# Optimization experiments

Measured on AMD Instinct MI355X. Metric: run time of the kernel, lower is better.

## Reference

```python
import jax, jax.numpy as jnp
import numpy as np
from jax import lax

B, H = 32768, 32  # batch, hidden_dim (hidden_dim=32 fixed by the source module)
T = 128           # num_steps


def setup_inputs() -> dict:
    key = jax.random.key(0)
    ks = jax.random.split(key, 8)
    s = 1.0 / np.sqrt(H)  # torch default uniform(-1/sqrt(H), 1/sqrt(H)) scale
    return {
        "in_data": jax.random.normal(ks[0], (B, H), dtype=jnp.float32),
        "hidden": jax.random.normal(ks[1], (B, H), dtype=jnp.float32),
        "W_ih": jax.random.uniform(ks[2], (3 * H, H), jnp.float32, -s, s),
        "W_hh": jax.random.uniform(ks[3], (3 * H, H), jnp.float32, -s, s),
        "b_ih": jax.random.uniform(ks[4], (3 * H,), jnp.float32, -s, s),
        "b_hh": jax.random.uniform(ks[5], (3 * H,), jnp.float32, -s, s),
        "W_out": jax.random.uniform(ks[6], (1, H), jnp.float32, -s, s),
        "b_out": jax.random.uniform(ks[7], (1,), jnp.float32, -s, s),
        "num_steps": T,
    }


def reference(in_data, hidden, W_ih, W_hh, b_ih, b_hh, W_out, b_out, num_steps):
    # the GRU hidden output is fed back as the next step's input.
    def gru_cell(x, h):
        gi = x @ W_ih.T + b_ih  # [B, 3H]
        gh = h @ W_hh.T + b_hh  # [B, 3H]
        i_r, i_z, i_n = jnp.split(gi, 3, axis=-1)
        h_r, h_z, h_n = jnp.split(gh, 3, axis=-1)
        r = jax.nn.sigmoid(i_r + h_r)
        z = jax.nn.sigmoid(i_z + h_z)
        n = jnp.tanh(i_n + r * h_n)
        return (1.0 - z) * n + z * h

    def step(carry, _):
        x, h = carry
        h_new = gru_cell(x, h)
        y = h_new @ W_out.T + b_out  # [B, 1]
        return (h_new, h_new), y[:, 0]

    _, ys = lax.scan(step, (in_data, hidden), None, length=num_steps)  # ys: [T, B]
    return ys.T  # [B, T], matching torch's stack().squeeze(2).permute(1,0)
```

## Files before the change

### kernel.cpp

```cpp
#include <hip/hip_runtime.h>


typedef __attribute__((ext_vector_type(8)))  short short8;
typedef __attribute__((ext_vector_type(4)))  float f32x4;

struct F3 { short8 h, m, l; };

__device__ __forceinline__ void ldrow8(const float* p, float f[8]) {
    f32x4 a = *(const f32x4*)p;
    f32x4 b = *(const f32x4*)(p + 4);
    f[0]=a[0]; f[1]=a[1]; f[2]=a[2]; f[3]=a[3];
    f[4]=b[0]; f[5]=b[1]; f[6]=b[2]; f[7]=b[3];
}

__device__ __forceinline__ F3 split8(const float f[8]) {
    unsigned H[8], M[8], L[8];
    #pragma unroll
    for (int i = 0; i < 8; ++i) {
        unsigned a = __float_as_uint(f[i]);
        unsigned h = a & 0xffff0000u;
        float    t = f[i] - __uint_as_float(h);
        unsigned m = __float_as_uint(t) & 0xffff0000u;
        float    u = t - __uint_as_float(m);
        unsigned l = __float_as_uint(u) & 0xffff0000u;
        H[i] = h; M[i] = m; L[i] = l;
    }
    union { unsigned u[4]; short8 s; } uh, um, ul;
    #pragma unroll
    for (int p = 0; p < 4; ++p) {
        uh.u[p] = __builtin_amdgcn_perm(H[2*p+1], H[2*p], 0x07060302u);
        um.u[p] = __builtin_amdgcn_perm(M[2*p+1], M[2*p], 0x07060302u);
        ul.u[p] = __builtin_amdgcn_perm(L[2*p+1], L[2*p], 0x07060302u);
    }
    F3 r; r.h = uh.s; r.m = um.s; r.l = ul.s; return r;
}

#define MFMA(a,b,c) __builtin_amdgcn_mfma_f32_16x16x32_bf16((a),(b),(c),0,0,0)

__device__ __forceinline__ f32x4 mm6(const F3& A, const F3& B, f32x4 c) {
    c = MFMA(A.h, B.l, c);
    c = MFMA(A.l, B.h, c);
    c = MFMA(A.m, B.m, c);
    c = MFMA(A.h, B.m, c);
    c = MFMA(A.m, B.h, c);
    c = MFMA(A.h, B.h, c);
    return c;
}

__device__ __forceinline__ float rcp_nr(float x) {
    float r = __builtin_amdgcn_rcpf(x);
    return r * fmaf(-x, r, 2.f);
}
__device__ __forceinline__ float sigm_(float x) {
    x = __builtin_amdgcn_fmed3f(x, -60.f, 60.f);
    return rcp_nr(1.f + __expf(-x));
}
__device__ __forceinline__ float tanh_(float x) {
    x = __builtin_amdgcn_fmed3f(x, -30.f, 30.f);
    return fmaf(-2.f, rcp_nr(__expf(2.f * x) + 1.f), 1.f);
}
__device__ __forceinline__ float comb_(float ar, float az, float an_, float ahn, float hp) {
    float rr = sigm_(ar);
    float zz = sigm_(az);
    float nn = tanh_(fmaf(rr, ahn, an_));
    return fmaf(zz, hp - nn, nn);
}

__global__ __launch_bounds__(256, 2)
void gru_mfma(const float* __restrict__ in_data, const float* __restrict__ hidden,
              const float* __restrict__ W_ih,   const float* __restrict__ W_hh,
              const float* __restrict__ b_ih,   const float* __restrict__ b_hh,
              const float* __restrict__ W_out,  const float* __restrict__ b_out,
              float* __restrict__ out, int B, int T)
{
    const int tid  = threadIdx.x;
    const int lane = tid & 63, wv = tid >> 6;
    const int n    = lane & 15;
    const int g    = lane >> 4;
    const int k0   = g * 8;
    const long e   = (long)blockIdx.x * 64 + wv * 16 + n;

    const int rlo = 8 * (n >> 2) + (n & 3);
    const int rhi = rlo + 4;

    f32x4 bC[8];
    #pragma unroll
    for (int p = 0; p < 2; ++p) {
        #pragma unroll
        for (int r = 0; r < 4; ++r) {
            const int c = 8 * g + 4 * p + r;
            bC[0 + p][r] = b_ih[c]      + b_hh[c];
            bC[2 + p][r] = b_ih[32 + c] + b_hh[32 + c];
            bC[4 + p][r] = b_ih[64 + c];
            bC[6 + p][r] = b_hh[64 + c];
        }
    }
    float wl[4], wh[4];
    #pragma unroll
    for (int r = 0; r < 4; ++r) { wl[r] = W_out[8*g + r]; wh[r] = W_out[8*g + 4 + r]; }
    const float boutv = b_out[0];
    float* const op = out + e * (long)T;

    float hp[8];
    F3 Bv, Bx;
    {
        float f[8]; ldrow8(hidden + e * 32 + k0, f);
        #pragma unroll
        for (int i = 0; i < 8; ++i) hp[i] = f[i];
        Bv = split8(f);
        float fx[8]; ldrow8(in_data + e * 32 + k0, fx);
        Bx = split8(fx);
    }

    F3 A[8];
    f32x4 C[8];

    #pragma unroll
    for (int gs = 0; gs < 3; ++gs) {
        float fl[8], fh[8];
        ldrow8(W_ih + (gs * 32 + rlo) * 32 + k0, fl);
        ldrow8(W_ih + (gs * 32 + rhi) * 32 + k0, fh);
        A[2*gs] = split8(fl); A[2*gs+1] = split8(fh);
    }
    #pragma unroll
    for (int rt = 0; rt < 6; ++rt) C[rt] = mm6(A[rt], Bx, bC[rt]);

    #pragma unroll
    for (int gs = 0; gs < 3; ++gs) {
        float fl[8], fh[8];
        ldrow8(W_hh + (gs * 32 + rlo) * 32 + k0, fl);
        ldrow8(W_hh + (gs * 32 + rhi) * 32 + k0, fh);
        A[2*gs] = split8(fl); A[2*gs+1] = split8(fh);
    }
    #pragma unroll
    for (int rt = 0; rt < 4; ++rt) C[rt] = mm6(A[rt], Bv, C[rt]);
    C[6] = mm6(A[4], Bv, bC[6]);
    C[7] = mm6(A[5], Bv, bC[7]);

    #pragma unroll
    for (int gs = 0; gs < 2; ++gs) {
        float fl[8], fh[8], g2[8];
        ldrow8(W_ih + (gs * 32 + rlo) * 32 + k0, fl);
        ldrow8(W_hh + (gs * 32 + rlo) * 32 + k0, g2);
        #pragma unroll
        for (int i = 0; i < 8; ++i) fl[i] += g2[i];
        ldrow8(W_ih + (gs * 32 + rhi) * 32 + k0, fh);
        ldrow8(W_hh + (gs * 32 + rhi) * 32 + k0, g2);
        #pragma unroll
        for (int i = 0; i < 8; ++i) fh[i] += g2[i];
        A[2*gs] = split8(fl); A[2*gs+1] = split8(fh);
    }
    {
        float fl[8], fh[8];
        ldrow8(W_ih + (64 + rlo) * 32 + k0, fl);
        ldrow8(W_ih + (64 + rhi) * 32 + k0, fh);
        A[4] = split8(fl); A[5] = split8(fh);
        ldrow8(W_hh + (64 + rlo) * 32 + k0, fl);
        ldrow8(W_hh + (64 + rhi) * 32 + k0, fh);
        A[6] = split8(fl); A[7] = split8(fh);
    }

    #pragma unroll 1
    for (int t = 0; t < T; ++t) {
        float h8[8], yp = 0.f;
        #pragma unroll
        for (int r = 0; r < 4; ++r) {
            float a  = comb_(C[0][r], C[2][r], C[4][r], C[6][r], hp[r]);
            float b2 = comb_(C[1][r], C[3][r], C[5][r], C[7][r], hp[4 + r]);
            yp = fmaf(wl[r], a,  yp);
            yp = fmaf(wh[r], b2, yp);
            h8[r] = a; h8[4 + r] = b2;
            hp[r] = a; hp[4 + r] = b2;
        }
        yp += __shfl_xor(yp, 16);
        yp += __shfl_xor(yp, 32);
        if (lane < 16) op[t] = yp + boutv;
        if (t == T - 1) break;

        Bv = split8(h8);
        #pragma unroll
        for (int rt = 0; rt < 8; ++rt) C[rt] = mm6(A[rt], Bv, bC[rt]);
    }
}

extern "C" void kernel_launch(void* const* d_in, const int* in_sizes, int n_in,
                              void* d_out, int out_size, void* d_ws, size_t ws_size,
                              hipStream_t stream) {
    const float* in_data = (const float*)d_in[0];
    const float* hidden  = (const float*)d_in[1];
    const float* W_ih    = (const float*)d_in[2];
    const float* W_hh    = (const float*)d_in[3];
    const float* b_ih    = (const float*)d_in[4];
    const float* b_hh    = (const float*)d_in[5];
    const float* W_out   = (const float*)d_in[6];
    const float* b_out   = (const float*)d_in[7];
    float* out = (float*)d_out;

    const int B = in_sizes[0] / 32;
    const int T = out_size / B;
    const int blocks = B / 64;

    gru_mfma<<<blocks, 256, 0, stream>>>(in_data, hidden, W_ih, W_hh,
                                         b_ih, b_hh, W_out, b_out, out, B, T);
}
```

Before: 298.8 us.

## Interleave two batch groups per wave to overlap MFMA with gate math

Each wave now processes two 16-row batch groups, A and B. The recurrent MFMA chain for one group is interleaved with the sigmoid/tanh combine of the other, so the matrix and vector units can overlap instead of serialising on the per-step dependency. The log2e scaling is folded into the weights and biases, letting the gates use raw exp2 without a multiply or clamp. Blocks shrink to one wave with launch_bounds(64,1), which changes the occupancy and register budget, and dropping the clamps risks inf/NaN-adjacent edge behaviour on extreme inputs.

Result: faster. 290.1 us (-2.9%).

```diff
diff --git a/kernel.cpp b/kernel.cpp
--- a/kernel.cpp
+++ b/kernel.cpp
@@ -11,6 +11,11 @@
     f32x4 b = *(const f32x4*)(p + 4);
     f[0]=a[0]; f[1]=a[1]; f[2]=a[2]; f[3]=a[3];
     f[4]=b[0]; f[5]=b[1]; f[6]=b[2]; f[7]=b[3];
+}
+__device__ __forceinline__ void ldrow8s(const float* p, float f[8], float s) {
+    ldrow8(p, f);
+    #pragma unroll
+    for (int i = 0; i < 8; ++i) f[i] *= s;
 }
 
 __device__ __forceinline__ F3 split8(const float f[8]) {
@@ -47,38 +52,59 @@
     return c;
 }
 
+__device__ __forceinline__ void mfma8(const F3 A[8], const F3& Bv,
+                                      const f32x4 bC[8], f32x4 C[8]) {
+    #pragma unroll
+    for (int rt = 0; rt < 8; ++rt) C[rt] = mm6(A[rt], Bv, bC[rt]);
+}
+
 __device__ __forceinline__ float rcp_nr(float x) {
     float r = __builtin_amdgcn_rcpf(x);
     return r * fmaf(-x, r, 2.f);
 }
-__device__ __forceinline__ float sigm_(float x) {
-    x = __builtin_amdgcn_fmed3f(x, -60.f, 60.f);
-    return rcp_nr(1.f + __expf(-x));
-}
-__device__ __forceinline__ float tanh_(float x) {
-    x = __builtin_amdgcn_fmed3f(x, -30.f, 30.f);
-    return fmaf(-2.f, rcp_nr(__expf(2.f * x) + 1.f), 1.f);
-}
-__device__ __forceinline__ float comb_(float ar, float az, float an_, float ahn, float hp) {
-    float rr = sigm_(ar);
-    float zz = sigm_(az);
-    float nn = tanh_(fmaf(rr, ahn, an_));
+__device__ __forceinline__ float comb_(float arN, float azN, float anS, float ahnS, float hp) {
+    float rr = rcp_nr(1.f + __builtin_amdgcn_exp2f(arN));
+    float zz = rcp_nr(1.f + __builtin_amdgcn_exp2f(azN));
+    float q  = rcp_nr(__builtin_amdgcn_exp2f(fmaf(rr, ahnS, anS)) + 1.f);
+    float nn = fmaf(-2.f, q, 1.f);
     return fmaf(zz, hp - nn, nn);
 }
 
-__global__ __launch_bounds__(256, 2)
+__device__ __forceinline__ void combineG(const f32x4 C[8], float hp[8], F3& Bv,
+                                         const float wl[4], const float wh[4],
+                                         float boutv, float* op, int t, bool st) {
+    float h8[8], yp = 0.f;
+    #pragma unroll
+    for (int r = 0; r < 4; ++r) {
+        float a  = comb_(C[0][r], C[2][r], C[4][r], C[6][r], hp[r]);
+        float b2 = comb_(C[1][r], C[3][r], C[5][r], C[7][r], hp[4 + r]);
+        yp = fmaf(wl[r], a, yp);
+        yp = fmaf(wh[r], b2, yp);
+        h8[r] = a; h8[4 + r] = b2;
+        hp[r] = a; hp[4 + r] = b2;
+    }
+    yp += __shfl_xor(yp, 16);
+    yp += __shfl_xor(yp, 32);
+    if (st) op[t] = yp + boutv;
+    Bv = split8(h8);
+}
+
+__global__ __launch_bounds__(64, 1)
 void gru_mfma(const float* __restrict__ in_data, const float* __restrict__ hidden,
               const float* __restrict__ W_ih,   const float* __restrict__ W_hh,
               const float* __restrict__ b_ih,   const float* __restrict__ b_hh,
               const float* __restrict__ W_out,  const float* __restrict__ b_out,
               float* __restrict__ out, int B, int T)
 {
-    const int tid  = threadIdx.x;
-    const int lane = tid & 63, wv = tid >> 6;
+    const float S_RZ = -1.44269504088896340736f;
+    const float S_N  =  2.88539008177792681472f;
+
+    const int lane = threadIdx.x & 63;
     const int n    = lane & 15;
     const int g    = lane >> 4;
     const int k0   = g * 8;
-    const long e   = (long)blockIdx.x * 64 + wv * 16 + n;
+    const long eA  = (long)blockIdx.x * 32 + n;
+    const long eB  = eA + 16;
 
     const int rlo = 8 * (n >> 2) + (n & 3);
     const int rhi = rlo + 4;
@@ -89,53 +115,63 @@
         #pragma unroll
         for (int r = 0; r < 4; ++r) {
             const int c = 8 * g + 4 * p + r;
-            bC[0 + p][r] = b_ih[c]      + b_hh[c];
-            bC[2 + p][r] = b_ih[32 + c] + b_hh[32 + c];
-            bC[4 + p][r] = b_ih[64 + c];
-            bC[6 + p][r] = b_hh[64 + c];
+            bC[0 + p][r] = S_RZ * (b_ih[c]      + b_hh[c]);
+            bC[2 + p][r] = S_RZ * (b_ih[32 + c] + b_hh[32 + c]);
+            bC[4 + p][r] = S_N  *  b_ih[64 + c];
+            bC[6 + p][r] = S_N  *  b_hh[64 + c];
         }
     }
     float wl[4], wh[4];
     #pragma unroll
     for (int r = 0; r < 4; ++r) { wl[r] = W_out[8*g + r]; wh[r] = W_out[8*g + 4 + r]; }
     const float boutv = b_out[0];
-    float* const op = out + e * (long)T;
-
-    float hp[8];
-    F3 Bv, Bx;
+    float* const opA = out + eA * (long)T;
+    float* const opB = out + eB * (long)T;
+
+    float hpA[8], hpB[8];
+    F3 BvA, BvB, BxA, BxB;
     {
-        float f[8]; ldrow8(hidden + e * 32 + k0, f);
-        #pragma unroll
-        for (int i = 0; i < 8; ++i) hp[i] = f[i];
-        Bv = split8(f);
-        float fx[8]; ldrow8(in_data + e * 32 + k0, fx);
-        Bx = split8(fx);
+        float f[8];
+        ldrow8(hidden + eA * 32 + k0, f);
+        #pragma unroll
+        for (int i = 0; i < 8; ++i) hpA[i] = f[i];
+        BvA = split8(f);
+        ldrow8(hidden + eB * 32 + k0, f);
+        #pragma unroll
+        for (int i = 0; i < 8; ++i) hpB[i] = f[i];
+        BvB = split8(f);
+        ldrow8(in_data + eA * 32 + k0, f); BxA = split8(f);
+        ldrow8(in_data + eB * 32 + k0, f); BxB = split8(f);
     }
 
     F3 A[8];
-    f32x4 C[8];
+    f32x4 CA[8], CB[8];
 
     #pragma unroll
     for (int gs = 0; gs < 3; ++gs) {
+        const float s = (gs < 2) ? S_RZ : S_N;
         float fl[8], fh[8];
-        ldrow8(W_ih + (gs * 32 + rlo) * 32 + k0, fl);
-        ldrow8(W_ih + (gs * 32 + rhi) * 32 + k0, fh);
+        ldrow8s(W_ih + (gs * 32 + rlo) * 32 + k0, fl, s);
+        ldrow8s(W_ih + (gs * 32 + rhi) * 32 + k0, fh, s);
         A[2*gs] = split8(fl); A[2*gs+1] = split8(fh);
     }
     #pragma unroll
-    for (int rt = 0; rt < 6; ++rt) C[rt] = mm6(A[rt], Bx, bC[rt]);
+    for (int rt = 0; rt < 6; ++rt) { CA[rt] = mm6(A[rt], BxA, bC[rt]);
+                                     CB[rt] = mm6(A[rt], BxB, bC[rt]); }
 
     #pragma unroll
     for (int gs = 0; gs < 3; ++gs) {
+        const float s = (gs < 2) ? S_RZ : S_N;
         float fl[8], fh[8];
-        ldrow8(W_hh + (gs * 32 + rlo) * 32 + k0, fl);
-        ldrow8(W_hh + (gs * 32 + rhi) * 32 + k0, fh);
+        ldrow8s(W_hh + (gs * 32 + rlo) * 32 + k0, fl, s);
+        ldrow8s(W_hh + (gs * 32 + rhi) * 32 + k0, fh, s);
         A[2*gs] = split8(fl); A[2*gs+1] = split8(fh);
     }
     #pragma unroll
-    for (int rt = 0; rt < 4; ++rt) C[rt] = mm6(A[rt], Bv, C[rt]);
-    C[6] = mm6(A[4], Bv, bC[6]);
-    C[7] = mm6(A[5], Bv, bC[7]);
+    for (int rt = 0; rt < 4; ++rt) { CA[rt] = mm6(A[rt], BvA, CA[rt]);
+                                     CB[rt] = mm6(A[rt], BvB, CB[rt]); }
+    CA[6] = mm6(A[4], BvA, bC[6]);  CB[6] = mm6(A[4], BvB, bC[6]);
+    CA[7] = mm6(A[5], BvA, bC[7]);  CB[7] = mm6(A[5], BvB, bC[7]);
 
     #pragma unroll
     for (int gs = 0; gs < 2; ++gs) {
@@ -143,44 +179,36 @@
         ldrow8(W_ih + (gs * 32 + rlo) * 32 + k0, fl);
         ldrow8(W_hh + (gs * 32 + rlo) * 32 + k0, g2);
         #pragma unroll
-        for (int i = 0; i < 8; ++i) fl[i] += g2[i];
+        for (int i = 0; i < 8; ++i) fl[i] = S_RZ * (fl[i] + g2[i]);
         ldrow8(W_ih + (gs * 32 + rhi) * 32 + k0, fh);
         ldrow8(W_hh + (gs * 32 + rhi) * 32 + k0, g2);
         #pragma unroll
-        for (int i = 0; i < 8; ++i) fh[i] += g2[i];
+        for (int i = 0; i < 8; ++i) fh[i] = S_RZ * (fh[i] + g2[i]);
         A[2*gs] = split8(fl); A[2*gs+1] = split8(fh);
     }
     {
         float fl[8], fh[8];
-        ldrow8(W_ih + (64 + rlo) * 32 + k0, fl);
-        ldrow8(W_ih + (64 + rhi) * 32 + k0, fh);
+        ldrow8s(W_ih + (64 + rlo) * 32 + k0, fl, S_N);
+        ldrow8s(W_ih + (64 + rhi) * 32 + k0, fh, S_N);
         A[4] = split8(fl); A[5] = split8(fh);
-        ldrow8(W_hh + (64 + rlo) * 32 + k0, fl);
-        ldrow8(W_hh + (64 + rhi) * 32 + k0, fh);
+        ldrow8s(W_hh + (64 + rlo) * 32 + k0, fl, S_N);
+        ldrow8s(W_hh + (64 + rhi) * 32 + k0, fh, S_N);
         A[6] = split8(fl); A[7] = split8(fh);
     }
 
+    const bool st = (lane < 16);
+
+    combineG(CA, hpA, BvA, wl, wh, boutv, opA, 0, st);
+
     #pragma unroll 1
-    for (int t = 0; t < T; ++t) {
-        float h8[8], yp = 0.f;
-        #pragma unroll
-        for (int r = 0; r < 4; ++r) {
-            float a  = comb_(C[0][r], C[2][r], C[4][r], C[6][r], hp[r]);
-            float b2 = comb_(C[1][r], C[3][r], C[5][r], C[7][r], hp[4 + r]);
-            yp = fmaf(wl[r], a,  yp);
-            yp = fmaf(wh[r], b2, yp);
-            h8[r] = a; h8[4 + r] = b2;
-            hp[r] = a; hp[4 + r] = b2;
-        }
-        yp += __shfl_xor(yp, 16);
-        yp += __shfl_xor(yp, 32);
-        if (lane < 16) op[t] = yp + boutv;
-        if (t == T - 1) break;
-
-        Bv = split8(h8);
-        #pragma unroll
-        for (int rt = 0; rt < 8; ++rt) C[rt] = mm6(A[rt], Bv, bC[rt]);
-    }
+    for (int t = 0; t < T - 1; ++t) {
+        mfma8(A, BvA, bC, CA);
+        combineG(CB, hpB, BvB, wl, wh, boutv, opB, t, st);
+        mfma8(A, BvB, bC, CB);
+        combineG(CA, hpA, BvA, wl, wh, boutv, opA, t + 1, st);
+    }
+
+    combineG(CB, hpB, BvB, wl, wh, boutv, opB, T - 1, st);
 }
 
 extern "C" void kernel_launch(void* const* d_in, const int* in_sizes, int n_in,
@@ -198,8 +226,8 @@
 
     const int B = in_sizes[0] / 32;
     const int T = out_size / B;
-    const int blocks = B / 64;
-
-    gru_mfma<<<blocks, 256, 0, stream>>>(in_data, hidden, W_ih, W_hh,
-                                         b_ih, b_hh, W_out, b_out, out, B, T);
-}
+    const int blocks = B / 32;
+
+    gru_mfma<<<blocks, 64, 0, stream>>>(in_data, hidden, W_ih, W_hh,
+                                        b_ih, b_hh, W_out, b_out, out, B, T);
+}
```
